# Performance work log

Measured on AMD Instinct MI355X. Metric: run time of the kernel, lower is better.

Reference implementation:

```python
import jax, jax.numpy as jnp
import numpy as np

B, L, D = 4, 4096, 128
WINDOW = 64
NEG = -1e9
LN_EPS = 1e-5


def setup_inputs() -> dict:
    key = jax.random.key(0)
    ks = jax.random.split(key, 6)
    x = jax.random.normal(ks[0], (B, L, D), dtype=jnp.float32)
    # windowed adjacency with self-loops: adj[b,i,j]=1 iff |i-j| <= WINDOW
    idx = jnp.arange(L)
    band = (jnp.abs(idx[:, None] - idx[None, :]) <= WINDOW).astype(jnp.int32)
    adj = jnp.broadcast_to(band, (B, L, L))
    mask = np.ones((B, L), dtype=np.int32)
    mask[B // 2 :, -L // 8 :] = 0
    mask = jnp.asarray(mask)
    s = 1.0 / np.sqrt(D)
    Wq = jax.random.normal(ks[1], (D, D), dtype=jnp.float32) * s
    Wk = jax.random.normal(ks[2], (D, D), dtype=jnp.float32) * s
    Wv = jax.random.normal(ks[3], (D, D), dtype=jnp.float32) * s
    W_upd = jax.random.normal(ks[4], (2 * D, D), dtype=jnp.float32) * (1.0 / np.sqrt(2 * D))
    b_upd = jnp.zeros((D,), dtype=jnp.float32)
    gamma = jnp.ones((D,), dtype=jnp.float32)
    beta = jnp.zeros((D,), dtype=jnp.float32)
    return {"x": x, "adj": adj, "mask": mask, "Wq": Wq, "Wk": Wk, "Wv": Wv,
            "W_upd": W_upd, "b_upd": b_upd, "gamma": gamma, "beta": beta}


def reference(x, adj, mask, Wq, Wk, Wv, W_upd, b_upd, gamma, beta):
    d = x.shape[-1]
    q = jnp.einsum("bld,de->ble", x, Wq)
    k = jnp.einsum("bld,de->ble", x, Wk)
    v = jnp.einsum("bld,de->ble", x, Wv)
    logits = jnp.einsum("bld,bmd->blm", q, k) / jnp.sqrt(jnp.float32(d))
    logits = jnp.where(adj == 0, NEG, logits)
    logits = jnp.where(mask[:, :, None] == 0, NEG, logits)
    logits = jnp.where(mask[:, None, :] == 0, NEG, logits)
    attn = jax.nn.softmax(logits, axis=-1)  # dropout = identity (eval mode)
    agg = jnp.einsum("blm,bmd->bld", attn, v)
    h = jnp.concatenate([x, agg], axis=-1)  # [B, L, 2D]
    upd = jax.nn.relu(h @ W_upd + b_upd)
    y = x + upd
    mu = jnp.mean(y, axis=-1, keepdims=True)
    var = jnp.var(y, axis=-1, keepdims=True)
    return gamma * (y - mu) * jax.lax.rsqrt(var + LN_EPS) + beta
```

## Files before the change

kernel.cpp:

```cpp
#include <hip/hip_runtime.h>

#define BB 4
#define LL 4096
#define DD 128
#define WIN 64
#define BL (BB * LL)

#define TQ 32
#define CK 64

__global__ __launch_bounds__(256) void qkv_kernel(
    const float* __restrict__ x, const float* __restrict__ Wq,
    const float* __restrict__ Wk, const float* __restrict__ Wv,
    float* __restrict__ q, float* __restrict__ k, float* __restrict__ v) {
  __shared__ float xs[32][132];
  __shared__ float ws[32][132];

  const int t = threadIdx.x;
  const int row0 = blockIdx.x * 32;
  const int tm = t >> 4;
  const int tn = t & 15;

  {
    int rr = t >> 5, d4 = t & 31;
    const float4* xg = (const float4*)(x + (size_t)row0 * DD);
    #pragma unroll
    for (int p = 0; p < 4; ++p) {
      int row = p * 8 + rr;
      ((float4*)&xs[row][0])[d4] = xg[row * 32 + d4];
    }
  }

  const float* Ws[3] = {Wq, Wk, Wv};
  float* outs[3] = {q, k, v};

  for (int w = 0; w < 3; ++w) {
    float acc0[8], acc1[8];
    #pragma unroll
    for (int j = 0; j < 8; ++j) { acc0[j] = 0.f; acc1[j] = 0.f; }

    for (int kc = 0; kc < 4; ++kc) {
      __syncthreads();
      {
        int rr = t >> 5, d4 = t & 31;
        const float4* wg = (const float4*)(Ws[w] + (size_t)kc * 32 * DD);
        #pragma unroll
        for (int p = 0; p < 4; ++p) {
          int row = p * 8 + rr;
          ((float4*)&ws[row][0])[d4] = wg[row * 32 + d4];
        }
      }
      __syncthreads();

      #pragma unroll
      for (int k4 = 0; k4 < 8; ++k4) {
        float4 a0 = ((const float4*)&xs[tm][0])[kc * 8 + k4];
        float4 a1 = ((const float4*)&xs[tm + 16][0])[kc * 8 + k4];
        float a0c[4] = {a0.x, a0.y, a0.z, a0.w};
        float a1c[4] = {a1.x, a1.y, a1.z, a1.w};
        #pragma unroll
        for (int o = 0; o < 4; ++o) {
          int kk = k4 * 4 + o;
          float4 b0 = ((const float4*)&ws[kk][0])[tn];
          float4 b1 = ((const float4*)&ws[kk][0])[16 + tn];
          acc0[0] += a0c[o] * b0.x; acc0[1] += a0c[o] * b0.y;
          acc0[2] += a0c[o] * b0.z; acc0[3] += a0c[o] * b0.w;
          acc0[4] += a0c[o] * b1.x; acc0[5] += a0c[o] * b1.y;
          acc0[6] += a0c[o] * b1.z; acc0[7] += a0c[o] * b1.w;
          acc1[0] += a1c[o] * b0.x; acc1[1] += a1c[o] * b0.y;
          acc1[2] += a1c[o] * b0.z; acc1[3] += a1c[o] * b0.w;
          acc1[4] += a1c[o] * b1.x; acc1[5] += a1c[o] * b1.y;
          acc1[6] += a1c[o] * b1.z; acc1[7] += a1c[o] * b1.w;
        }
      }
    }
    float* op = outs[w] + (size_t)row0 * DD;
    ((float4*)(op + (size_t)tm * DD))[tn] =
        make_float4(acc0[0], acc0[1], acc0[2], acc0[3]);
    ((float4*)(op + (size_t)tm * DD))[16 + tn] =
        make_float4(acc0[4], acc0[5], acc0[6], acc0[7]);
    ((float4*)(op + (size_t)(tm + 16) * DD))[tn] =
        make_float4(acc1[0], acc1[1], acc1[2], acc1[3]);
    ((float4*)(op + (size_t)(tm + 16) * DD))[16 + tn] =
        make_float4(acc1[4], acc1[5], acc1[6], acc1[7]);
  }
}

__global__ __launch_bounds__(128) void vmean_kernel(
    const float* __restrict__ v, float* __restrict__ vmean_sum) {
  const int b = blockIdx.x >> 6;
  const int seg = blockIdx.x & 63;
  const int d = threadIdx.x;
  const float* vb = v + ((size_t)b * LL + seg * 64) * DD;
  float acc = 0.f;
  for (int l = 0; l < 64; ++l) acc += vb[(size_t)l * DD + d];
  atomicAdd(&vmean_sum[b * DD + d], acc);
}

__global__ __launch_bounds__(128) void attn_kernel(
    const float* __restrict__ q, const float* __restrict__ k,
    const float* __restrict__ v, const float* __restrict__ vmean_sum,
    const int* __restrict__ mask, float* __restrict__ agg) {
  __shared__ float qs[TQ][132];
  __shared__ float ks[CK][132];
  __shared__ float ps[TQ][68];
  __shared__ int cms[CK];

  const int bx = blockIdx.x;
  const int b = bx >> 7;
  const int i0 = (bx & 127) * TQ;
  const int t = threadIdx.x;
  const int tm = t >> 4;
  const int tn = t & 15;

  const size_t rowbase = ((size_t)b * LL + i0) * DD;

  {
    int rr = t >> 5, d4 = t & 31;
    const float4* qg = (const float4*)(q + rowbase);
    #pragma unroll
    for (int p = 0; p < 8; ++p) {
      int row = p * 4 + rr;
      ((float4*)&qs[row][0])[d4] = qg[row * 32 + d4];
    }
  }

  float accv[4][8];
  float lsum[4];
  #pragma unroll
  for (int m = 0; m < 4; ++m) {
    lsum[m] = 0.f;
    #pragma unroll
    for (int j = 0; j < 8; ++j) accv[m][j] = 0.f;
  }

  for (int ch = 0; ch < 3; ++ch) {
    const int j0 = i0 - WIN + ch * CK;
    __syncthreads();
    {
      int rr = t >> 5, d4 = t & 31;
      #pragma unroll
      for (int p = 0; p < 16; ++p) {
        int row = p * 4 + rr;
        int j = j0 + row;
        int jc = j < 0 ? 0 : (j > LL - 1 ? LL - 1 : j);
        ((float4*)&ks[row][0])[d4] =
            ((const float4*)(k + ((size_t)b * LL + jc) * DD))[d4];
      }
      if (t < CK) {
        int j = j0 + t;
        cms[t] = (j >= 0 && j < LL) ? mask[b * LL + j] : 0;
      }
    }
    __syncthreads();

    float S[4][4];
    #pragma unroll
    for (int m = 0; m < 4; ++m)
      #pragma unroll
      for (int n = 0; n < 4; ++n) S[m][n] = 0.f;

    for (int k4 = 0; k4 < 32; ++k4) {
      float4 a[4], bb[4];
      #pragma unroll
      for (int m = 0; m < 4; ++m)
        a[m] = ((const float4*)&qs[tm + 8 * m][0])[k4];
      #pragma unroll
      for (int n = 0; n < 4; ++n)
        bb[n] = ((const float4*)&ks[tn + 16 * n][0])[k4];
      #pragma unroll
      for (int m = 0; m < 4; ++m)
        #pragma unroll
        for (int n = 0; n < 4; ++n)
          S[m][n] += a[m].x * bb[n].x + a[m].y * bb[n].y + a[m].z * bb[n].z +
                     a[m].w * bb[n].w;
    }

    #pragma unroll
    for (int m = 0; m < 4; ++m) {
      int iR = i0 + tm + 8 * m;
      #pragma unroll
      for (int n = 0; n < 4; ++n) {
        int col = tn + 16 * n;
        int j = j0 + col;
        int dj = iR - j;
        dj = dj < 0 ? -dj : dj;
        bool ok = (dj <= WIN) && ((unsigned)j < (unsigned)LL) && (cms[col] != 0);
        float p = ok ? __expf(S[m][n] * 0.08838834764831845f) : 0.f;
        lsum[m] += p;
        ps[tm + 8 * m][col] = p;
      }
    }
    __syncthreads();

    {
      int rr = t >> 5, d4 = t & 31;
      #pragma unroll
      for (int p = 0; p < 16; ++p) {
        int row = p * 4 + rr;
        int j = j0 + row;
        int jc = j < 0 ? 0 : (j > LL - 1 ? LL - 1 : j);
        ((float4*)&ks[row][0])[d4] =
            ((const float4*)(v + ((size_t)b * LL + jc) * DD))[d4];
      }
    }
    __syncthreads();

    #pragma unroll 2
    for (int c = 0; c < CK; ++c) {
      float pm[4];
      #pragma unroll
      for (int m = 0; m < 4; ++m) pm[m] = ps[tm + 8 * m][c];
      float4 v0 = ((const float4*)&ks[c][0])[tn];
      float4 v1 = ((const float4*)&ks[c][0])[16 + tn];
      #pragma unroll
      for (int m = 0; m < 4; ++m) {
        accv[m][0] += pm[m] * v0.x; accv[m][1] += pm[m] * v0.y;
        accv[m][2] += pm[m] * v0.z; accv[m][3] += pm[m] * v0.w;
        accv[m][4] += pm[m] * v1.x; accv[m][5] += pm[m] * v1.y;
        accv[m][6] += pm[m] * v1.z; accv[m][7] += pm[m] * v1.w;
      }
    }
  }

  #pragma unroll
  for (int m = 0; m < 4; ++m) {
    float l = lsum[m];
    l += __shfl_xor(l, 1);
    l += __shfl_xor(l, 2);
    l += __shfl_xor(l, 4);
    l += __shfl_xor(l, 8);
    lsum[m] = l;
  }

  #pragma unroll
  for (int m = 0; m < 4; ++m) {
    int row = tm + 8 * m;
    int iR = i0 + row;
    float inv = 1.0f / lsum[m];
    float4 o0, o1;
    if (mask[b * LL + iR] != 0) {
      o0 = make_float4(accv[m][0] * inv, accv[m][1] * inv, accv[m][2] * inv,
                       accv[m][3] * inv);
      o1 = make_float4(accv[m][4] * inv, accv[m][5] * inv, accv[m][6] * inv,
                       accv[m][7] * inv);
    } else {
      const float4* vm = (const float4*)(vmean_sum + b * DD);
      float4 m0 = vm[tn], m1 = vm[16 + tn];
      const float s = 1.0f / LL;
      o0 = make_float4(m0.x * s, m0.y * s, m0.z * s, m0.w * s);
      o1 = make_float4(m1.x * s, m1.y * s, m1.z * s, m1.w * s);
    }
    ((float4*)(agg + rowbase + (size_t)row * DD))[tn] = o0;
    ((float4*)(agg + rowbase + (size_t)row * DD))[16 + tn] = o1;
  }
}

__global__ __launch_bounds__(256) void mlp_ln_kernel(
    const float* __restrict__ x, const float* __restrict__ agg,
    const float* __restrict__ Wu, const float* __restrict__ bias,
    const float* __restrict__ gamma, const float* __restrict__ beta,
    float* __restrict__ out) {
  __shared__ float hs[32][36];
  __shared__ float ws[32][132];

  const int t = threadIdx.x;
  const int row0 = blockIdx.x * 32;
  const int tm = t >> 4, tn = t & 15;

  float acc0[8], acc1[8];
  #pragma unroll
  for (int j = 0; j < 8; ++j) { acc0[j] = 0.f; acc1[j] = 0.f; }

  for (int kc = 0; kc < 8; ++kc) {
    __syncthreads();
    {
      const float* src = (kc < 4) ? (x + (size_t)row0 * DD + kc * 32)
                                  : (agg + (size_t)row0 * DD + (kc - 4) * 32);
      int row = t >> 3, d4 = t & 7;
      ((float4*)&hs[row][0])[d4] = ((const float4*)(src + (size_t)row * DD))[d4];
    }
    {
      int rr = t >> 5, d4 = t & 31;
      const float4* wg = (const float4*)(Wu + (size_t)kc * 32 * DD);
      #pragma unroll
      for (int p = 0; p < 4; ++p) {
        int row = p * 8 + rr;
        ((float4*)&ws[row][0])[d4] = wg[row * 32 + d4];
      }
    }
    __syncthreads();

    #pragma unroll
    for (int k4 = 0; k4 < 8; ++k4) {
      float4 a0 = ((const float4*)&hs[tm][0])[k4];
      float4 a1 = ((const float4*)&hs[tm + 16][0])[k4];
      float a0c[4] = {a0.x, a0.y, a0.z, a0.w};
      float a1c[4] = {a1.x, a1.y, a1.z, a1.w};
      #pragma unroll
      for (int o = 0; o < 4; ++o) {
        int kk = k4 * 4 + o;
        float4 b0 = ((const float4*)&ws[kk][0])[tn];
        float4 b1 = ((const float4*)&ws[kk][0])[16 + tn];
        acc0[0] += a0c[o] * b0.x; acc0[1] += a0c[o] * b0.y;
        acc0[2] += a0c[o] * b0.z; acc0[3] += a0c[o] * b0.w;
        acc0[4] += a0c[o] * b1.x; acc0[5] += a0c[o] * b1.y;
        acc0[6] += a0c[o] * b1.z; acc0[7] += a0c[o] * b1.w;
        acc1[0] += a1c[o] * b0.x; acc1[1] += a1c[o] * b0.y;
        acc1[2] += a1c[o] * b0.z; acc1[3] += a1c[o] * b0.w;
        acc1[4] += a1c[o] * b1.x; acc1[5] += a1c[o] * b1.y;
        acc1[6] += a1c[o] * b1.z; acc1[7] += a1c[o] * b1.w;
      }
    }
  }

  const float4 bv0 = ((const float4*)bias)[tn];
  const float4 bv1 = ((const float4*)bias)[16 + tn];
  const float4 g0 = ((const float4*)gamma)[tn];
  const float4 g1 = ((const float4*)gamma)[16 + tn];
  const float4 be0 = ((const float4*)beta)[tn];
  const float4 be1 = ((const float4*)beta)[16 + tn];

  #pragma unroll
  for (int m = 0; m < 2; ++m) {
    const float* accp0 = m ? acc1 : acc0;
    int row = tm + 16 * m;
    const float4 xr0 = ((const float4*)(x + (size_t)(row0 + row) * DD))[tn];
    const float4 xr1 = ((const float4*)(x + (size_t)(row0 + row) * DD))[16 + tn];
    float y[8];
    y[0] = xr0.x + fmaxf(accp0[0] + bv0.x, 0.f);
    y[1] = xr0.y + fmaxf(accp0[1] + bv0.y, 0.f);
    y[2] = xr0.z + fmaxf(accp0[2] + bv0.z, 0.f);
    y[3] = xr0.w + fmaxf(accp0[3] + bv0.w, 0.f);
    y[4] = xr1.x + fmaxf(accp0[4] + bv1.x, 0.f);
    y[5] = xr1.y + fmaxf(accp0[5] + bv1.y, 0.f);
    y[6] = xr1.z + fmaxf(accp0[6] + bv1.z, 0.f);
    y[7] = xr1.w + fmaxf(accp0[7] + bv1.w, 0.f);
    float s = 0.f, ss = 0.f;
    #pragma unroll
    for (int j = 0; j < 8; ++j) { s += y[j]; ss += y[j] * y[j]; }
    s += __shfl_xor(s, 1); ss += __shfl_xor(ss, 1);
    s += __shfl_xor(s, 2); ss += __shfl_xor(ss, 2);
    s += __shfl_xor(s, 4); ss += __shfl_xor(ss, 4);
    s += __shfl_xor(s, 8); ss += __shfl_xor(ss, 8);
    float mu = s * (1.0f / DD);
    float var = ss * (1.0f / DD) - mu * mu;
    float rstd = rsqrtf(var + 1e-5f);
    float4 o0 = make_float4(g0.x * ((y[0] - mu) * rstd) + be0.x,
                            g0.y * ((y[1] - mu) * rstd) + be0.y,
                            g0.z * ((y[2] - mu) * rstd) + be0.z,
                            g0.w * ((y[3] - mu) * rstd) + be0.w);
    float4 o1 = make_float4(g1.x * ((y[4] - mu) * rstd) + be1.x,
                            g1.y * ((y[5] - mu) * rstd) + be1.y,
                            g1.z * ((y[6] - mu) * rstd) + be1.z,
                            g1.w * ((y[7] - mu) * rstd) + be1.w);
    ((float4*)(out + (size_t)(row0 + row) * DD))[tn] = o0;
    ((float4*)(out + (size_t)(row0 + row) * DD))[16 + tn] = o1;
  }
}

extern "C" void kernel_launch(void* const* d_in, const int* in_sizes, int n_in,
                              void* d_out, int out_size, void* d_ws,
                              size_t ws_size, hipStream_t stream) {
  const float* x = (const float*)d_in[0];
  const int* mask = (const int*)d_in[2];
  const float* Wq = (const float*)d_in[3];
  const float* Wk = (const float*)d_in[4];
  const float* Wv = (const float*)d_in[5];
  const float* Wu = (const float*)d_in[6];
  const float* bias = (const float*)d_in[7];
  const float* gamma = (const float*)d_in[8];
  const float* beta = (const float*)d_in[9];
  float* out = (float*)d_out;

  float* q = (float*)d_ws;
  float* k = q + (size_t)BL * DD;
  float* v = k + (size_t)BL * DD;
  float* agg = v + (size_t)BL * DD;
  float* vmean_sum = agg + (size_t)BL * DD;

  hipMemsetAsync(vmean_sum, 0, BB * DD * sizeof(float), stream);

  qkv_kernel<<<BL / 32, 256, 0, stream>>>(x, Wq, Wk, Wv, q, k, v);
  vmean_kernel<<<BB * 64, 128, 0, stream>>>(v, vmean_sum);
  attn_kernel<<<BL / TQ, 128, 0, stream>>>(q, k, v, vmean_sum, mask, agg);
  mlp_ln_kernel<<<BL / 32, 256, 0, stream>>>(x, agg, Wu, bias, gamma, beta,
                                             out);
}
```

Before: 422.3 us.

## Store Q/K/V as bf16 and fuse V column sum into QKV kernel

Measured after the change: 429.9 us. Within noise of the previous version (+1.8%).

```diff
diff --git a/kernel.cpp b/kernel.cpp
--- a/kernel.cpp
+++ b/kernel.cpp
@@ -9,10 +9,36 @@
 #define TQ 32
 #define CK 64
 
+typedef unsigned short u16;
+
+__device__ __forceinline__ u16 f2b(float f) {
+  union { float f; unsigned int u; } x;
+  x.f = f;
+  unsigned int r = x.u + 0x7fffu + ((x.u >> 16) & 1u);
+  return (u16)(r >> 16);
+}
+__device__ __forceinline__ float b2f_lo(unsigned int u) {
+  union { unsigned int u; float f; } x;
+  x.u = u << 16;
+  return x.f;
+}
+__device__ __forceinline__ float b2f_hi(unsigned int u) {
+  union { unsigned int u; float f; } x;
+  x.u = u & 0xffff0000u;
+  return x.f;
+}
+__device__ __forceinline__ void unpack8(uint4 u, float* f) {
+  f[0] = b2f_lo(u.x); f[1] = b2f_hi(u.x);
+  f[2] = b2f_lo(u.y); f[3] = b2f_hi(u.y);
+  f[4] = b2f_lo(u.z); f[5] = b2f_hi(u.z);
+  f[6] = b2f_lo(u.w); f[7] = b2f_hi(u.w);
+}
+
 __global__ __launch_bounds__(256) void qkv_kernel(
     const float* __restrict__ x, const float* __restrict__ Wq,
     const float* __restrict__ Wk, const float* __restrict__ Wv,
-    float* __restrict__ q, float* __restrict__ k, float* __restrict__ v) {
+    u16* __restrict__ q, u16* __restrict__ k, u16* __restrict__ v,
+    float* __restrict__ vmean_sum) {
   __shared__ float xs[32][132];
   __shared__ float ws[32][132];
 
@@ -32,7 +58,7 @@
   }
 
   const float* Ws[3] = {Wq, Wk, Wv};
-  float* outs[3] = {q, k, v};
+  u16* outs[3] = {q, k, v};
 
   for (int w = 0; w < 3; ++w) {
     float acc0[8], acc1[8];
@@ -74,36 +100,44 @@
         }
       }
     }
-    float* op = outs[w] + (size_t)row0 * DD;
-    ((float4*)(op + (size_t)tm * DD))[tn] =
-        make_float4(acc0[0], acc0[1], acc0[2], acc0[3]);
-    ((float4*)(op + (size_t)tm * DD))[16 + tn] =
-        make_float4(acc0[4], acc0[5], acc0[6], acc0[7]);
-    ((float4*)(op + (size_t)(tm + 16) * DD))[tn] =
-        make_float4(acc1[0], acc1[1], acc1[2], acc1[3]);
-    ((float4*)(op + (size_t)(tm + 16) * DD))[16 + tn] =
-        make_float4(acc1[4], acc1[5], acc1[6], acc1[7]);
-  }
-}
-
-__global__ __launch_bounds__(128) void vmean_kernel(
-    const float* __restrict__ v, float* __restrict__ vmean_sum) {
-  const int b = blockIdx.x >> 6;
-  const int seg = blockIdx.x & 63;
-  const int d = threadIdx.x;
-  const float* vb = v + ((size_t)b * LL + seg * 64) * DD;
-  float acc = 0.f;
-  for (int l = 0; l < 64; ++l) acc += vb[(size_t)l * DD + d];
-  atomicAdd(&vmean_sum[b * DD + d], acc);
+
+    u16* op = outs[w] + (size_t)row0 * DD;
+    {
+      ushort4 s;
+      s.x = f2b(acc0[0]); s.y = f2b(acc0[1]); s.z = f2b(acc0[2]); s.w = f2b(acc0[3]);
+      *(ushort4*)(op + (size_t)tm * DD + 4 * tn) = s;
+      s.x = f2b(acc0[4]); s.y = f2b(acc0[5]); s.z = f2b(acc0[6]); s.w = f2b(acc0[7]);
+      *(ushort4*)(op + (size_t)tm * DD + 64 + 4 * tn) = s;
+      s.x = f2b(acc1[0]); s.y = f2b(acc1[1]); s.z = f2b(acc1[2]); s.w = f2b(acc1[3]);
+      *(ushort4*)(op + (size_t)(tm + 16) * DD + 4 * tn) = s;
+      s.x = f2b(acc1[4]); s.y = f2b(acc1[5]); s.z = f2b(acc1[6]); s.w = f2b(acc1[7]);
+      *(ushort4*)(op + (size_t)(tm + 16) * DD + 64 + 4 * tn) = s;
+    }
+
+    if (w == 2) {
+      __syncthreads();
+      ((float4*)&ws[tm][0])[tn] = make_float4(acc0[0], acc0[1], acc0[2], acc0[3]);
+      ((float4*)&ws[tm][0])[16 + tn] = make_float4(acc0[4], acc0[5], acc0[6], acc0[7]);
+      ((float4*)&ws[tm + 16][0])[tn] = make_float4(acc1[0], acc1[1], acc1[2], acc1[3]);
+      ((float4*)&ws[tm + 16][0])[16 + tn] = make_float4(acc1[4], acc1[5], acc1[6], acc1[7]);
+      __syncthreads();
+      if (t < DD) {
+        float s = 0.f;
+        #pragma unroll 8
+        for (int r = 0; r < 32; ++r) s += ws[r][t];
+        atomicAdd(&vmean_sum[(row0 >> 12) * DD + t], s);
+      }
+    }
+  }
 }
 
 __global__ __launch_bounds__(128) void attn_kernel(
-    const float* __restrict__ q, const float* __restrict__ k,
-    const float* __restrict__ v, const float* __restrict__ vmean_sum,
+    const u16* __restrict__ q, const u16* __restrict__ k,
+    const u16* __restrict__ v, const float* __restrict__ vmean_sum,
     const int* __restrict__ mask, float* __restrict__ agg) {
-  __shared__ float qs[TQ][132];
-  __shared__ float ks[CK][132];
-  __shared__ float ps[TQ][68];
+  __shared__ u16 qs[TQ][136];
+  __shared__ u16 ks[CK][136];
+  __shared__ float ps[TQ][66];
   __shared__ int cms[CK];
 
   const int bx = blockIdx.x;
@@ -116,12 +150,11 @@
   const size_t rowbase = ((size_t)b * LL + i0) * DD;
 
   {
-    int rr = t >> 5, d4 = t & 31;
-    const float4* qg = (const float4*)(q + rowbase);
-    #pragma unroll
-    for (int p = 0; p < 8; ++p) {
-      int row = p * 4 + rr;
-      ((float4*)&qs[row][0])[d4] = qg[row * 32 + d4];
+    const uint4* qg = (const uint4*)(q + rowbase);
+    #pragma unroll
+    for (int p = 0; p < 4; ++p) {
+      int row = p * 8 + tm;
+      *(uint4*)&qs[row][8 * tn] = qg[row * 16 + tn];
     }
   }
 
@@ -137,15 +170,15 @@
   for (int ch = 0; ch < 3; ++ch) {
     const int j0 = i0 - WIN + ch * CK;
     __syncthreads();
+
     {
-      int rr = t >> 5, d4 = t & 31;
-      #pragma unroll
-      for (int p = 0; p < 16; ++p) {
-        int row = p * 4 + rr;
+      #pragma unroll
+      for (int p = 0; p < 8; ++p) {
+        int row = p * 8 + tm;
         int j = j0 + row;
         int jc = j < 0 ? 0 : (j > LL - 1 ? LL - 1 : j);
-        ((float4*)&ks[row][0])[d4] =
-            ((const float4*)(k + ((size_t)b * LL + jc) * DD))[d4];
+        *(uint4*)&ks[row][8 * tn] =
+            ((const uint4*)(k + ((size_t)b * LL + jc) * DD))[tn];
       }
       if (t < CK) {
         int j = j0 + t;
@@ -160,20 +193,23 @@
       #pragma unroll
       for (int n = 0; n < 4; ++n) S[m][n] = 0.f;
 
-    for (int k4 = 0; k4 < 32; ++k4) {
-      float4 a[4], bb[4];
+    for (int k8 = 0; k8 < 16; ++k8) {
+      float af[4][8], bf[4][8];
       #pragma unroll
       for (int m = 0; m < 4; ++m)
-        a[m] = ((const float4*)&qs[tm + 8 * m][0])[k4];
+        unpack8(*(const uint4*)&qs[tm + 8 * m][8 * k8], af[m]);
       #pragma unroll
       for (int n = 0; n < 4; ++n)
-        bb[n] = ((const float4*)&ks[tn + 16 * n][0])[k4];
+        unpack8(*(const uint4*)&ks[tn + 16 * n][8 * k8], bf[n]);
       #pragma unroll
       for (int m = 0; m < 4; ++m)
         #pragma unroll
-        for (int n = 0; n < 4; ++n)
-          S[m][n] += a[m].x * bb[n].x + a[m].y * bb[n].y + a[m].z * bb[n].z +
-                     a[m].w * bb[n].w;
+        for (int n = 0; n < 4; ++n) {
+          float s = S[m][n];
+          #pragma unroll
+          for (int j = 0; j < 8; ++j) s += af[m][j] * bf[n][j];
+          S[m][n] = s;
+        }
     }
 
     #pragma unroll
@@ -194,32 +230,28 @@
     __syncthreads();
 
     {
-      int rr = t >> 5, d4 = t & 31;
-      #pragma unroll
-      for (int p = 0; p < 16; ++p) {
-        int row = p * 4 + rr;
+      #pragma unroll
+      for (int p = 0; p < 8; ++p) {
+        int row = p * 8 + tm;
         int j = j0 + row;
         int jc = j < 0 ? 0 : (j > LL - 1 ? LL - 1 : j);
-        ((float4*)&ks[row][0])[d4] =
-            ((const float4*)(v + ((size_t)b * LL + jc) * DD))[d4];
+        *(uint4*)&ks[row][8 * tn] =
+            ((const uint4*)(v + ((size_t)b * LL + jc) * DD))[tn];
       }
     }
     __syncthreads();
 
     #pragma unroll 2
     for (int c = 0; c < CK; ++c) {
+      float vf[8];
+      unpack8(*(const uint4*)&ks[c][8 * tn], vf);
       float pm[4];
       #pragma unroll
       for (int m = 0; m < 4; ++m) pm[m] = ps[tm + 8 * m][c];
-      float4 v0 = ((const float4*)&ks[c][0])[tn];
-      float4 v1 = ((const float4*)&ks[c][0])[16 + tn];
-      #pragma unroll
-      for (int m = 0; m < 4; ++m) {
-        accv[m][0] += pm[m] * v0.x; accv[m][1] += pm[m] * v0.y;
-        accv[m][2] += pm[m] * v0.z; accv[m][3] += pm[m] * v0.w;
-        accv[m][4] += pm[m] * v1.x; accv[m][5] += pm[m] * v1.y;
-        accv[m][6] += pm[m] * v1.z; accv[m][7] += pm[m] * v1.w;
-      }
+      #pragma unroll
+      for (int m = 0; m < 4; ++m)
+        #pragma unroll
+        for (int j = 0; j < 8; ++j) accv[m][j] += pm[m] * vf[j];
     }
   }
 
@@ -237,22 +269,19 @@
   for (int m = 0; m < 4; ++m) {
     int row = tm + 8 * m;
     int iR = i0 + row;
-    float inv = 1.0f / lsum[m];
-    float4 o0, o1;
+    float o[8];
     if (mask[b * LL + iR] != 0) {
-      o0 = make_float4(accv[m][0] * inv, accv[m][1] * inv, accv[m][2] * inv,
-                       accv[m][3] * inv);
-      o1 = make_float4(accv[m][4] * inv, accv[m][5] * inv, accv[m][6] * inv,
-                       accv[m][7] * inv);
+      float inv = 1.0f / lsum[m];
+      #pragma unroll
+      for (int j = 0; j < 8; ++j) o[j] = accv[m][j] * inv;
     } else {
-      const float4* vm = (const float4*)(vmean_sum + b * DD);
-      float4 m0 = vm[tn], m1 = vm[16 + tn];
       const float s = 1.0f / LL;
-      o0 = make_float4(m0.x * s, m0.y * s, m0.z * s, m0.w * s);
-      o1 = make_float4(m1.x * s, m1.y * s, m1.z * s, m1.w * s);
-    }
-    ((float4*)(agg + rowbase + (size_t)row * DD))[tn] = o0;
-    ((float4*)(agg + rowbase + (size_t)row * DD))[16 + tn] = o1;
+      #pragma unroll
+      for (int j = 0; j < 8; ++j) o[j] = vmean_sum[b * DD + 8 * tn + j] * s;
+    }
+    float* dst = agg + rowbase + (size_t)row * DD + 8 * tn;
+    *(float4*)dst = make_float4(o[0], o[1], o[2], o[3]);
+    *(float4*)(dst + 4) = make_float4(o[4], o[5], o[6], o[7]);
   }
 }
 
@@ -373,16 +402,15 @@
   const float* beta = (const float*)d_in[9];
   float* out = (float*)d_out;
 
-  float* q = (float*)d_ws;
-  float* k = q + (size_t)BL * DD;
-  float* v = k + (size_t)BL * DD;
-  float* agg = v + (size_t)BL * DD;
-  float* vmean_sum = agg + (size_t)BL * DD;
+  float* agg = (float*)d_ws;
+  u16* q = (u16*)(agg + (size_t)BL * DD);
+  u16* k = q + (size_t)BL * DD;
+  u16* v = k + (size_t)BL * DD;
+  float* vmean_sum = (float*)(v + (size_t)BL * DD);
 
   hipMemsetAsync(vmean_sum, 0, BB * DD * sizeof(float), stream);
 
-  qkv_kernel<<<BL / 32, 256, 0, stream>>>(x, Wq, Wk, Wv, q, k, v);
-  vmean_kernel<<<BB * 64, 128, 0, stream>>>(v, vmean_sum);
+  qkv_kernel<<<BL / 32, 256, 0, stream>>>(x, Wq, Wk, Wv, q, k, v, vmean_sum);
   attn_kernel<<<BL / TQ, 128, 0, stream>>>(q, k, v, vmean_sum, mask, agg);
   mlp_ln_kernel<<<BL / 32, 256, 0, stream>>>(x, agg, Wu, bias, gamma, beta,
                                              out);
```
